# Optimization experiments

Hardware: AMD Instinct MI355X
Metric: run time of the kernel (lower is better)

Reference implementation:

```python
import jax, jax.numpy as jnp
import numpy as np

N, IN_F, OUT_F = 1024, 256, 1024

def setup_inputs() -> dict:
    key = jax.random.key(0)
    k1, k2 = jax.random.split(key)
    x = jax.random.normal(k1, (N, IN_F), dtype=jnp.float32)
    centres = jax.random.normal(k2, (OUT_F, IN_F), dtype=jnp.float32)  # normal_(0,1) init
    log_sigmas = jnp.zeros((OUT_F,), dtype=jnp.float32)  # constant_(0) init
    return {"x": x, "centres": centres, "log_sigmas": log_sigmas}

def reference(x, centres, log_sigmas):
    # diff: (N, out_features, in_features) broadcast, matching torch expand
    diff = x[:, None, :] - centres[None, :, :]
    # Euclidean distance then per-centre sigma scaling: (N, out_features)
    distances = jnp.sqrt(jnp.sum(diff * diff, axis=-1)) / jnp.exp(log_sigmas)[None, :]
    # gaussian basis function: exp(-0.5 * d^2)
    return jnp.exp(-0.5 * distances * distances)
```

## Files before the change

kernel.cpp:

```cpp
#include <hip/hip_runtime.h>
#include <math.h>

#define K_FEAT 256
#define M_OUT  1024
#define N_ROWS 1024

#define TM 64
#define TN 32
#define LSTR 264

typedef short bf16x8 __attribute__((ext_vector_type(8)));
typedef float f32x4  __attribute__((ext_vector_type(4)));

__global__ __launch_bounds__(256, 2) void rbf_mfma(
    const float* __restrict__ x,
    const float* __restrict__ centres,
    const float* __restrict__ log_sigmas,
    float* __restrict__ out)
{
    __shared__ unsigned short xs[TM * LSTR];
    __shared__ unsigned short cs[TN * LSTR];
    __shared__ float nx[TM];
    __shared__ float nc[TN];

    const int tid  = threadIdx.x;
    const int lane = tid & 63;
    const int wave = tid >> 6;
    const int row_base = blockIdx.y * TM;
    const int col_base = blockIdx.x * TN;

    #pragma unroll
    for (int l = 0; l < 12; ++l) {
        const int  li    = (l < 8) ? l : (l - 8);
        const int  chunk = tid + li * 256;
        const int  row   = chunk >> 5;
        const int  k0    = (chunk & 31) * 8;
        const float* src = (l < 8)
            ? (x       + (size_t)(row_base + row) * K_FEAT + k0)
            : (centres + (size_t)(col_base + row) * K_FEAT + k0);
        const float4 v0 = ((const float4*)src)[0];
        const float4 v1 = ((const float4*)src)[1];
        uint4 p;
        p.x = (__float_as_uint(v0.x) >> 16) | (__float_as_uint(v0.y) & 0xffff0000u);
        p.y = (__float_as_uint(v0.z) >> 16) | (__float_as_uint(v0.w) & 0xffff0000u);
        p.z = (__float_as_uint(v1.x) >> 16) | (__float_as_uint(v1.y) & 0xffff0000u);
        p.w = (__float_as_uint(v1.z) >> 16) | (__float_as_uint(v1.w) & 0xffff0000u);
        unsigned short* dst = (l < 8) ? &xs[row * LSTR + k0] : &cs[row * LSTR + k0];
        *(uint4*)dst = p;
    }
    __syncthreads();

    if (tid < TM + TN) {
        const unsigned short* src = (tid < TM) ? &xs[tid * LSTR] : &cs[(tid - TM) * LSTR];
        float s0 = 0.f, s1 = 0.f, s2 = 0.f, s3 = 0.f;
        #pragma unroll
        for (int k = 0; k < K_FEAT; k += 8) {
            const uint4 q = *(const uint4*)(src + k);
            const float f0 = __uint_as_float(q.x << 16);
            const float f1 = __uint_as_float(q.x & 0xffff0000u);
            const float f2 = __uint_as_float(q.y << 16);
            const float f3 = __uint_as_float(q.y & 0xffff0000u);
            const float f4 = __uint_as_float(q.z << 16);
            const float f5 = __uint_as_float(q.z & 0xffff0000u);
            const float f6 = __uint_as_float(q.w << 16);
            const float f7 = __uint_as_float(q.w & 0xffff0000u);
            s0 = fmaf(f0, f0, s0); s1 = fmaf(f1, f1, s1);
            s2 = fmaf(f2, f2, s2); s3 = fmaf(f3, f3, s3);
            s0 = fmaf(f4, f4, s0); s1 = fmaf(f5, f5, s1);
            s2 = fmaf(f6, f6, s2); s3 = fmaf(f7, f7, s3);
        }
        const float s = (s0 + s1) + (s2 + s3);
        if (tid < TM) nx[tid] = s; else nc[tid - TM] = s;
    }

    const int m    = lane & 15;
    const int quad = lane >> 4;
    const int row_slab = wave * 16;
    f32x4 acc0 = {0.f, 0.f, 0.f, 0.f};
    f32x4 acc1 = {0.f, 0.f, 0.f, 0.f};
    const unsigned short* ap  = &xs[(row_slab + m) * LSTR + quad * 8];
    const unsigned short* bp0 = &cs[ m       * LSTR + quad * 8];
    const unsigned short* bp1 = &cs[(16 + m) * LSTR + quad * 8];
    #pragma unroll
    for (int kk = 0; kk < 8; ++kk) {
        const bf16x8 a  = *(const bf16x8*)(ap  + kk * 32);
        const bf16x8 b0 = *(const bf16x8*)(bp0 + kk * 32);
        const bf16x8 b1 = *(const bf16x8*)(bp1 + kk * 32);
        acc0 = __builtin_amdgcn_mfma_f32_16x16x32_bf16(a, b0, acc0, 0, 0, 0);
        acc1 = __builtin_amdgcn_mfma_f32_16x16x32_bf16(a, b1, acc1, 0, 0, 0);
    }
    __syncthreads();

    const int col0 = col_base + m;
    const int col1 = col_base + 16 + m;
    const float i2s0 = __expf(-2.0f * log_sigmas[col0]);
    const float i2s1 = __expf(-2.0f * log_sigmas[col1]);
    const float ncv0 = nc[m];
    const float ncv1 = nc[16 + m];
    #pragma unroll
    for (int i = 0; i < 4; ++i) {
        const int r = row_slab + quad * 4 + i;
        const float nxv = nx[r];
        const float d0 = nxv + ncv0 - 2.0f * acc0[i];
        const float d1 = nxv + ncv1 - 2.0f * acc1[i];
        float* o = out + (size_t)(row_base + r) * M_OUT;
        o[col0] = __expf(-0.5f * d0 * i2s0);
        o[col1] = __expf(-0.5f * d1 * i2s1);
    }
}

extern "C" void kernel_launch(void* const* d_in, const int* in_sizes, int n_in,
                              void* d_out, int out_size, void* d_ws, size_t ws_size,
                              hipStream_t stream) {
    const float* x  = (const float*)d_in[0];
    const float* c  = (const float*)d_in[1];
    const float* ls = (const float*)d_in[2];
    float* out = (float*)d_out;

    dim3 grid(M_OUT / TN, N_ROWS / TM);
    rbf_mfma<<<grid, dim3(256), 0, stream>>>(x, c, ls, out);
}
```

Baseline: 62.38 us.

## Precompute fp32 row norms in separate kernel and shrink tile to 32x32

Adds a separate kernel that computes squared norms of x rows and centres in full fp32 into workspace, removing the in-block serial norm loop and its extra barrier. The main kernel's tile shrinks from 64x32 to 32x32, with each wave computing one 16x16 MFMA tile, doubling the grid and raising the occupancy hint to 4. This trades an extra launch and more redundant centre loads for more parallelism. It also changes the norms from bf16-derived to fp32 values.

After: 63.17 us. No clear change (+1.3%).

```diff
diff --git a/kernel.cpp b/kernel.cpp
--- a/kernel.cpp
+++ b/kernel.cpp
@@ -5,23 +5,38 @@
 #define M_OUT  1024
 #define N_ROWS 1024
 
-#define TM 64
+#define TM 32
 #define TN 32
 #define LSTR 264
 
 typedef short bf16x8 __attribute__((ext_vector_type(8)));
 typedef float f32x4  __attribute__((ext_vector_type(4)));
 
-__global__ __launch_bounds__(256, 2) void rbf_mfma(
+__global__ __launch_bounds__(256) void row_norms(
+    const float* __restrict__ x, const float* __restrict__ c,
+    float* __restrict__ norms)
+{
+    const int lane = threadIdx.x & 63;
+    const int wave = threadIdx.x >> 6;
+    const int row  = blockIdx.x * 4 + wave;
+    const float* src = (row < N_ROWS) ? (x + (size_t)row * K_FEAT)
+                                      : (c + (size_t)(row - N_ROWS) * K_FEAT);
+    const float4 v = ((const float4*)src)[lane];
+    float s = v.x * v.x + v.y * v.y + v.z * v.z + v.w * v.w;
+    #pragma unroll
+    for (int off = 32; off; off >>= 1) s += __shfl_down(s, off, 64);
+    if (lane == 0) norms[row] = s;
+}
+
+__global__ __launch_bounds__(256, 4) void rbf_mfma(
     const float* __restrict__ x,
     const float* __restrict__ centres,
     const float* __restrict__ log_sigmas,
+    const float* __restrict__ norms,
     float* __restrict__ out)
 {
     __shared__ unsigned short xs[TM * LSTR];
     __shared__ unsigned short cs[TN * LSTR];
-    __shared__ float nx[TM];
-    __shared__ float nc[TN];
 
     const int tid  = threadIdx.x;
     const int lane = tid & 63;
@@ -30,12 +45,12 @@
     const int col_base = blockIdx.x * TN;
 
     #pragma unroll
-    for (int l = 0; l < 12; ++l) {
-        const int  li    = (l < 8) ? l : (l - 8);
+    for (int l = 0; l < 8; ++l) {
+        const int  li    = l & 3;
         const int  chunk = tid + li * 256;
         const int  row   = chunk >> 5;
         const int  k0    = (chunk & 31) * 8;
-        const float* src = (l < 8)
+        const float* src = (l < 4)
             ? (x       + (size_t)(row_base + row) * K_FEAT + k0)
             : (centres + (size_t)(col_base + row) * K_FEAT + k0);
         const float4 v0 = ((const float4*)src)[0];
@@ -45,67 +60,34 @@
         p.y = (__float_as_uint(v0.z) >> 16) | (__float_as_uint(v0.w) & 0xffff0000u);
         p.z = (__float_as_uint(v1.x) >> 16) | (__float_as_uint(v1.y) & 0xffff0000u);
         p.w = (__float_as_uint(v1.z) >> 16) | (__float_as_uint(v1.w) & 0xffff0000u);
-        unsigned short* dst = (l < 8) ? &xs[row * LSTR + k0] : &cs[row * LSTR + k0];
+        unsigned short* dst = (l < 4) ? &xs[row * LSTR + k0] : &cs[row * LSTR + k0];
         *(uint4*)dst = p;
     }
     __syncthreads();
 
-    if (tid < TM + TN) {
-        const unsigned short* src = (tid < TM) ? &xs[tid * LSTR] : &cs[(tid - TM) * LSTR];
-        float s0 = 0.f, s1 = 0.f, s2 = 0.f, s3 = 0.f;
-        #pragma unroll
-        for (int k = 0; k < K_FEAT; k += 8) {
-            const uint4 q = *(const uint4*)(src + k);
-            const float f0 = __uint_as_float(q.x << 16);
-            const float f1 = __uint_as_float(q.x & 0xffff0000u);
-            const float f2 = __uint_as_float(q.y << 16);
-            const float f3 = __uint_as_float(q.y & 0xffff0000u);
-            const float f4 = __uint_as_float(q.z << 16);
-            const float f5 = __uint_as_float(q.z & 0xffff0000u);
-            const float f6 = __uint_as_float(q.w << 16);
-            const float f7 = __uint_as_float(q.w & 0xffff0000u);
-            s0 = fmaf(f0, f0, s0); s1 = fmaf(f1, f1, s1);
-            s2 = fmaf(f2, f2, s2); s3 = fmaf(f3, f3, s3);
-            s0 = fmaf(f4, f4, s0); s1 = fmaf(f5, f5, s1);
-            s2 = fmaf(f6, f6, s2); s3 = fmaf(f7, f7, s3);
-        }
-        const float s = (s0 + s1) + (s2 + s3);
-        if (tid < TM) nx[tid] = s; else nc[tid - TM] = s;
+    const int m    = lane & 15;
+    const int quad = lane >> 4;
+    const int tr   = (wave & 1) * 16;
+    const int tc   = (wave >> 1) * 16;
+    f32x4 acc = {0.f, 0.f, 0.f, 0.f};
+    const unsigned short* ap = &xs[(tr + m) * LSTR + quad * 8];
+    const unsigned short* bp = &cs[(tc + m) * LSTR + quad * 8];
+    #pragma unroll
+    for (int kk = 0; kk < 8; ++kk) {
+        const bf16x8 a = *(const bf16x8*)(ap + kk * 32);
+        const bf16x8 b = *(const bf16x8*)(bp + kk * 32);
+        acc = __builtin_amdgcn_mfma_f32_16x16x32_bf16(a, b, acc, 0, 0, 0);
     }
 
-    const int m    = lane & 15;
-    const int quad = lane >> 4;
-    const int row_slab = wave * 16;
-    f32x4 acc0 = {0.f, 0.f, 0.f, 0.f};
-    f32x4 acc1 = {0.f, 0.f, 0.f, 0.f};
-    const unsigned short* ap  = &xs[(row_slab + m) * LSTR + quad * 8];
-    const unsigned short* bp0 = &cs[ m       * LSTR + quad * 8];
-    const unsigned short* bp1 = &cs[(16 + m) * LSTR + quad * 8];
-    #pragma unroll
-    for (int kk = 0; kk < 8; ++kk) {
-        const bf16x8 a  = *(const bf16x8*)(ap  + kk * 32);
-        const bf16x8 b0 = *(const bf16x8*)(bp0 + kk * 32);
-        const bf16x8 b1 = *(const bf16x8*)(bp1 + kk * 32);
-        acc0 = __builtin_amdgcn_mfma_f32_16x16x32_bf16(a, b0, acc0, 0, 0, 0);
-        acc1 = __builtin_amdgcn_mfma_f32_16x16x32_bf16(a, b1, acc1, 0, 0, 0);
-    }
-    __syncthreads();
-
-    const int col0 = col_base + m;
-    const int col1 = col_base + 16 + m;
-    const float i2s0 = __expf(-2.0f * log_sigmas[col0]);
-    const float i2s1 = __expf(-2.0f * log_sigmas[col1]);
-    const float ncv0 = nc[m];
-    const float ncv1 = nc[16 + m];
+    const int   col = col_base + tc + m;
+    const float i2s = __expf(-2.0f * log_sigmas[col]);
+    const float ncv = norms[N_ROWS + col];
     #pragma unroll
     for (int i = 0; i < 4; ++i) {
-        const int r = row_slab + quad * 4 + i;
-        const float nxv = nx[r];
-        const float d0 = nxv + ncv0 - 2.0f * acc0[i];
-        const float d1 = nxv + ncv1 - 2.0f * acc1[i];
-        float* o = out + (size_t)(row_base + r) * M_OUT;
-        o[col0] = __expf(-0.5f * d0 * i2s0);
-        o[col1] = __expf(-0.5f * d1 * i2s1);
+        const int   r   = tr + quad * 4 + i;
+        const float nxv = norms[row_base + r];
+        const float d2  = nxv + ncv - 2.0f * acc[i];
+        out[(size_t)(row_base + r) * M_OUT + col] = __expf(-0.5f * d2 * i2s);
     }
 }
 
@@ -115,8 +97,10 @@
     const float* x  = (const float*)d_in[0];
     const float* c  = (const float*)d_in[1];
     const float* ls = (const float*)d_in[2];
-    float* out = (float*)d_out;
+    float* out   = (float*)d_out;
+    float* norms = (float*)d_ws;
 
+    row_norms<<<dim3(2 * N_ROWS / 4), dim3(256), 0, stream>>>(x, c, norms);
     dim3 grid(M_OUT / TN, N_ROWS / TM);
-    rbf_mfma<<<grid, dim3(256), 0, stream>>>(x, c, ls, out);
+    rbf_mfma<<<grid, dim3(256), 0, stream>>>(x, c, ls, norms, out);
 }
```

## Fuse squared-norm computation into global load loop via wave shuffles

Applied to the files above, without the earlier changes.

Squared norms of x and centre rows are now computed from the fp32 values during the global-to-LDS load. Each load is one float4 per thread and a 16-lane shuffle reduction produces partial norms, which replaces the separate serial per-row norm pass over bf16 LDS data that ran on only 96 threads. The trailing barrier is removed and the epilogue folds the -0.5 factor into the norms. Norms are now taken from fp32 rather than bf16-rounded values, which changes numerics slightly, and the load loop issues more, smaller loads.

Result: slower. 68.10 us (+9.2%).

```diff
diff --git a/kernel.cpp b/kernel.cpp
--- a/kernel.cpp
+++ b/kernel.cpp
@@ -12,7 +12,7 @@
 typedef short bf16x8 __attribute__((ext_vector_type(8)));
 typedef float f32x4  __attribute__((ext_vector_type(4)));
 
-__global__ __launch_bounds__(256, 2) void rbf_mfma(
+__global__ __launch_bounds__(256, 2) void rbf_fused(
     const float* __restrict__ x,
     const float* __restrict__ centres,
     const float* __restrict__ log_sigmas,
@@ -20,65 +20,43 @@
 {
     __shared__ unsigned short xs[TM * LSTR];
     __shared__ unsigned short cs[TN * LSTR];
-    __shared__ float nx[TM];
-    __shared__ float nc[TN];
+    __shared__ float nrm4[TM + TN][4];
 
     const int tid  = threadIdx.x;
     const int lane = tid & 63;
-    const int wave = tid >> 6;
     const int row_base = blockIdx.y * TM;
     const int col_base = blockIdx.x * TN;
 
     #pragma unroll
-    for (int l = 0; l < 12; ++l) {
-        const int  li    = (l < 8) ? l : (l - 8);
-        const int  chunk = tid + li * 256;
-        const int  row   = chunk >> 5;
-        const int  k0    = (chunk & 31) * 8;
-        const float* src = (l < 8)
+    for (int l = 0; l < 24; ++l) {
+        const int row = 4 * l + (tid >> 6);
+        const int k0  = (tid & 63) * 4;
+        const bool isx = row < TM;
+        const float* src = isx
             ? (x       + (size_t)(row_base + row) * K_FEAT + k0)
-            : (centres + (size_t)(col_base + row) * K_FEAT + k0);
-        const float4 v0 = ((const float4*)src)[0];
-        const float4 v1 = ((const float4*)src)[1];
-        uint4 p;
-        p.x = (__float_as_uint(v0.x) >> 16) | (__float_as_uint(v0.y) & 0xffff0000u);
-        p.y = (__float_as_uint(v0.z) >> 16) | (__float_as_uint(v0.w) & 0xffff0000u);
-        p.z = (__float_as_uint(v1.x) >> 16) | (__float_as_uint(v1.y) & 0xffff0000u);
-        p.w = (__float_as_uint(v1.z) >> 16) | (__float_as_uint(v1.w) & 0xffff0000u);
-        unsigned short* dst = (l < 8) ? &xs[row * LSTR + k0] : &cs[row * LSTR + k0];
-        *(uint4*)dst = p;
+            : (centres + (size_t)(col_base + row - TM) * K_FEAT + k0);
+        const float4 v = *(const float4*)src;
+        uint2 p;
+        p.x = (__float_as_uint(v.x) >> 16) | (__float_as_uint(v.y) & 0xffff0000u);
+        p.y = (__float_as_uint(v.z) >> 16) | (__float_as_uint(v.w) & 0xffff0000u);
+        unsigned short* dst = isx ? &xs[row * LSTR + k0] : &cs[(row - TM) * LSTR + k0];
+        *(uint2*)dst = p;
+        float s = 0.5f * (v.x * v.x + v.y * v.y + v.z * v.z + v.w * v.w);
+        s += __shfl_down(s, 8, 16);
+        s += __shfl_down(s, 4, 16);
+        s += __shfl_down(s, 2, 16);
+        s += __shfl_down(s, 1, 16);
+        if ((lane & 15) == 0) nrm4[row][lane >> 4] = s;
     }
     __syncthreads();
 
-    if (tid < TM + TN) {
-        const unsigned short* src = (tid < TM) ? &xs[tid * LSTR] : &cs[(tid - TM) * LSTR];
-        float s0 = 0.f, s1 = 0.f, s2 = 0.f, s3 = 0.f;
-        #pragma unroll
-        for (int k = 0; k < K_FEAT; k += 8) {
-            const uint4 q = *(const uint4*)(src + k);
-            const float f0 = __uint_as_float(q.x << 16);
-            const float f1 = __uint_as_float(q.x & 0xffff0000u);
-            const float f2 = __uint_as_float(q.y << 16);
-            const float f3 = __uint_as_float(q.y & 0xffff0000u);
-            const float f4 = __uint_as_float(q.z << 16);
-            const float f5 = __uint_as_float(q.z & 0xffff0000u);
-            const float f6 = __uint_as_float(q.w << 16);
-            const float f7 = __uint_as_float(q.w & 0xffff0000u);
-            s0 = fmaf(f0, f0, s0); s1 = fmaf(f1, f1, s1);
-            s2 = fmaf(f2, f2, s2); s3 = fmaf(f3, f3, s3);
-            s0 = fmaf(f4, f4, s0); s1 = fmaf(f5, f5, s1);
-            s2 = fmaf(f6, f6, s2); s3 = fmaf(f7, f7, s3);
-        }
-        const float s = (s0 + s1) + (s2 + s3);
-        if (tid < TM) nx[tid] = s; else nc[tid - TM] = s;
-    }
-
+    const int wave = tid >> 6;
     const int m    = lane & 15;
     const int quad = lane >> 4;
-    const int row_slab = wave * 16;
+    const int slab = wave * 16;
     f32x4 acc0 = {0.f, 0.f, 0.f, 0.f};
     f32x4 acc1 = {0.f, 0.f, 0.f, 0.f};
-    const unsigned short* ap  = &xs[(row_slab + m) * LSTR + quad * 8];
+    const unsigned short* ap  = &xs[(slab + m) * LSTR + quad * 8];
     const unsigned short* bp0 = &cs[ m       * LSTR + quad * 8];
     const unsigned short* bp1 = &cs[(16 + m) * LSTR + quad * 8];
     #pragma unroll
@@ -89,23 +67,23 @@
         acc0 = __builtin_amdgcn_mfma_f32_16x16x32_bf16(a, b0, acc0, 0, 0, 0);
         acc1 = __builtin_amdgcn_mfma_f32_16x16x32_bf16(a, b1, acc1, 0, 0, 0);
     }
-    __syncthreads();
 
     const int col0 = col_base + m;
     const int col1 = col_base + 16 + m;
-    const float i2s0 = __expf(-2.0f * log_sigmas[col0]);
-    const float i2s1 = __expf(-2.0f * log_sigmas[col1]);
-    const float ncv0 = nc[m];
-    const float ncv1 = nc[16 + m];
+    const float sc0 = __expf(-2.0f * log_sigmas[col0]);
+    const float sc1 = __expf(-2.0f * log_sigmas[col1]);
+    const f32x4 q0 = *(const f32x4*)nrm4[TM + m];
+    const f32x4 q1 = *(const f32x4*)nrm4[TM + 16 + m];
+    const float h0 = (q0[0] + q0[1]) + (q0[2] + q0[3]);
+    const float h1 = (q1[0] + q1[1]) + (q1[2] + q1[3]);
     #pragma unroll
     for (int i = 0; i < 4; ++i) {
-        const int r = row_slab + quad * 4 + i;
-        const float nxv = nx[r];
-        const float d0 = nxv + ncv0 - 2.0f * acc0[i];
-        const float d1 = nxv + ncv1 - 2.0f * acc1[i];
+        const int   r  = slab + quad * 4 + i;
+        const f32x4 qx = *(const f32x4*)nrm4[r];
+        const float hx = (qx[0] + qx[1]) + (qx[2] + qx[3]);
         float* o = out + (size_t)(row_base + r) * M_OUT;
-        o[col0] = __expf(-0.5f * d0 * i2s0);
-        o[col1] = __expf(-0.5f * d1 * i2s1);
+        o[col0] = __expf((acc0[i] - hx - h0) * sc0);
+        o[col1] = __expf((acc1[i] - hx - h1) * sc1);
     }
 }
 
@@ -118,5 +96,5 @@
     float* out = (float*)d_out;
 
     dim3 grid(M_OUT / TN, N_ROWS / TM);
-    rbf_mfma<<<grid, dim3(256), 0, stream>>>(x, c, ls, out);
+    rbf_fused<<<grid, dim3(256), 0, stream>>>(x, c, ls, out);
 }
```
